# Kernel optimization log

Measured on AMD Instinct MI355X. Metric: run time of the kernel, lower is better.

## Reference

```python
import jax, jax.numpy as jnp
import numpy as np

IM_SIZE = (128, 128)  # N_i per image dim
N_BATCH, N_COILS, N_TRJ = 1, 8, 8192


def _image_grid(im_size):
    # r_i in [-1/2, 1/2): (arange(N_i) - N_i//2) / N_i, flattened to (R, d)
    axes = [(jnp.arange(n, dtype=jnp.float32) - n // 2) / n for n in im_size]
    mesh = jnp.meshgrid(*axes, indexing='ij')
    return jnp.stack([m.reshape(-1) for m in mesh], axis=-1)  # (R, d)


def setup_inputs() -> dict:
    key = jax.random.key(0)
    k1, k2, k3 = jax.random.split(key, 3)
    img_real = jax.random.normal(k1, (N_BATCH, N_COILS) + IM_SIZE, dtype=jnp.float32)
    img_imag = jax.random.normal(k2, (N_BATCH, N_COILS) + IM_SIZE, dtype=jnp.float32)
    # trajectory k_i uniform in [-N_i/2, N_i/2]
    scale = jnp.asarray(IM_SIZE, dtype=jnp.float32)
    trj = (jax.random.uniform(k3, (N_BATCH, N_TRJ, len(IM_SIZE)), dtype=jnp.float32) - 0.5) * scale
    return {"img_real": img_real, "img_imag": img_imag, "trj": trj}


def reference(img_real, img_imag, trj):
    # matrix_nufft.forward: ksp[n,c,k] = sum_r img[n,c,r] * exp(-j 2 pi k . r)
    d = trj.shape[-1]
    im_size = img_real.shape[-d:]
    grid = _image_grid(im_size)                              # (R, d)
    phase = jnp.einsum('nkd,rd->nkr', trj, grid)             # (N, K, R)
    A = jnp.exp(-2j * jnp.pi * phase)                        # (N, K, R) complex64
    img = (img_real + 1j * img_imag).reshape(img_real.shape[0], -1, grid.shape[0])  # (N, C, R)
    ksp = jnp.einsum('nkr,ncr->nck', A, img)                 # (N, C, K) complex64
    # return real/imag stacked on last axis (harness-friendly real output)
    return jnp.stack([ksp.real, ksp.imag], axis=-1)          # (N, C, K, 2)
```

## Files before the change

### kernel.cpp

```cpp
#include <hip/hip_runtime.h>
#include <math.h>


#define K_TOTAL 8192
#define KB      64
#define NX      128
#define NY      128

typedef short  bf16x8 __attribute__((ext_vector_type(8)));
typedef float  f32x4  __attribute__((ext_vector_type(4)));

__device__ inline unsigned short f32_to_bf16_rne(float f) {
    unsigned int u = __float_as_uint(f);
    u += 0x7FFFu + ((u >> 16) & 1u);
    return (unsigned short)(u >> 16);
}
__device__ inline unsigned pack2(float a, float b) {
    return (unsigned)f32_to_bf16_rne(a) | ((unsigned)f32_to_bf16_rne(b) << 16);
}

__global__ __launch_bounds__(512, 1) void nufft_mfma_kernel(
    const float* __restrict__ imgR,
    const float* __restrict__ imgI,
    const float* __restrict__ trj,
    float* __restrict__ out)
{
    __shared__ __align__(16) unsigned short slab[2][2][128 * 128];

    const int tid = threadIdx.x;
    const int bid = blockIdx.x;
    const int cg  = bid >> 7;
    const int kg0 = (bid & 127) * KB;
    const int c0  = cg * 2;

    const int wave = tid >> 6;
    const int lane = tid & 63;
    const int l15  = lane & 15;
    const int lg   = lane >> 4;
    const int c2   = wave & 1;
    const int kq   = wave >> 1;
    const int c    = c0 + c2;

    const int rowgrp = tid >> 5;
    const int seg    = tid & 31;

    {
        float4 L0[4], L1[4];
        const float* bR0 = imgR + (c0 * NX) * NY + seg * 4;
        const float* bI0 = imgI + (c0 * NX) * NY + seg * 4;
        const float* bR1 = imgR + ((c0 + 1) * NX) * NY + seg * 4;
        const float* bI1 = imgI + ((c0 + 1) * NX) * NY + seg * 4;

        {
            const int row = rowgrp;
            L0[0] = *(const float4*)(bR0 + row * NY);
            L0[1] = *(const float4*)(bI0 + row * NY);
            L0[2] = *(const float4*)(bR1 + row * NY);
            L0[3] = *(const float4*)(bI1 + row * NY);
        }
#pragma unroll
        for (int i = 0; i < 8; ++i) {
            float4* cu = (i & 1) ? L1 : L0;
            float4* nx = (i & 1) ? L0 : L1;
            if (i < 7) {
                const int row = rowgrp + 16 * (i + 1);
                nx[0] = *(const float4*)(bR0 + row * NY);
                nx[1] = *(const float4*)(bI0 + row * NY);
                nx[2] = *(const float4*)(bR1 + row * NY);
                nx[3] = *(const float4*)(bI1 + row * NY);
            }
            const int row = rowgrp + 16 * i;
            const int off = row * 256 + ((seg * 8) ^ ((row & 15) << 4));
            uint2 v;
            v.x = pack2(cu[0].x, cu[0].y); v.y = pack2(cu[0].z, cu[0].w);
            *(uint2*)((char*)&slab[0][0][0] + off) = v;
            v.x = pack2(cu[1].x, cu[1].y); v.y = pack2(cu[1].z, cu[1].w);
            *(uint2*)((char*)&slab[0][1][0] + off) = v;
            v.x = pack2(cu[2].x, cu[2].y); v.y = pack2(cu[2].z, cu[2].w);
            *(uint2*)((char*)&slab[1][0][0] + off) = v;
            v.x = pack2(cu[3].x, cu[3].y); v.y = pack2(cu[3].z, cu[3].w);
            *(uint2*)((char*)&slab[1][1][0] + off) = v;
        }
    }

    bf16x8 aR[4], aI[4];
    {
        const float ky = trj[(kg0 + kq * 16 + l15) * 2 + 1];
        float u = -ky * (1.0f / 128.0f); u -= floorf(u);
        float s1i, s1r; __sincosf(6.283185307179586f * u, &s1i, &s1r);
#pragma unroll
        for (int ys = 0; ys < 4; ++ys) {
            const int y0 = ys * 32 + lg * 8;
            float t = -ky * (float)(y0 - 64) * (1.0f / 128.0f); t -= floorf(t);
            float ci_, cr_; __sincosf(6.283185307179586f * t, &ci_, &cr_);
#pragma unroll
            for (int m = 0; m < 8; ++m) {
                aR[ys][m] = (short)f32_to_bf16_rne(cr_);
                aI[ys][m] = (short)f32_to_bf16_rne(ci_);
                const float nr = cr_ * s1r - ci_ * s1i;
                ci_ = cr_ * s1i + ci_ * s1r;
                cr_ = nr;
            }
        }
    }

    float kxv[4];
#pragma unroll
    for (int j = 0; j < 4; ++j)
        kxv[j] = trj[(kg0 + kq * 16 + lg * 4 + j) * 2 + 0];

    __syncthreads();

    const char* sbR = (const char*)&slab[c2][0][0];
    const char* sbI = (const char*)&slab[c2][1][0];

    f32x4 outRe = {0,0,0,0};
    f32x4 outIm = {0,0,0,0};

#pragma unroll
    for (int nt = 0; nt < 8; ++nt) {
        const int x    = nt * 16 + l15;
        const int rowb = x * 256;

        f32x4 P = {0,0,0,0}, Q = {0,0,0,0}, U = {0,0,0,0}, V = {0,0,0,0};
#pragma unroll
        for (int ys = 0; ys < 4; ++ys) {
            const int inb = (lg * 16 + ys * 64) ^ (l15 << 4);
            const bf16x8 bR = *(const bf16x8*)(sbR + rowb + inb);
            const bf16x8 bI = *(const bf16x8*)(sbI + rowb + inb);
            P = __builtin_amdgcn_mfma_f32_16x16x32_bf16(aR[ys], bR, P, 0, 0, 0);
            Q = __builtin_amdgcn_mfma_f32_16x16x32_bf16(aI[ys], bI, Q, 0, 0, 0);
            U = __builtin_amdgcn_mfma_f32_16x16x32_bf16(aR[ys], bI, U, 0, 0, 0);
            V = __builtin_amdgcn_mfma_f32_16x16x32_bf16(aI[ys], bR, V, 0, 0, 0);
        }

        const float rx = (float)(x - 64) * (1.0f / 128.0f);
#pragma unroll
        for (int j = 0; j < 4; ++j) {
            float t = -kxv[j] * rx; t -= floorf(t);
            float eI_, eR_; __sincosf(6.283185307179586f * t, &eI_, &eR_);
            const float TR = P[j] - Q[j];
            const float TI = U[j] + V[j];
            outRe[j] += eR_ * TR - eI_ * TI;
            outIm[j] += eR_ * TI + eI_ * TR;
        }
    }

#pragma unroll
    for (int j = 0; j < 4; ++j) {
        float r_ = outRe[j];
        float i_ = outIm[j];
#pragma unroll
        for (int m = 1; m < 16; m <<= 1) {
            r_ += __shfl_xor(r_, m, 64);
            i_ += __shfl_xor(i_, m, 64);
        }
        if (l15 == 0) {
            const int kg = kg0 + kq * 16 + lg * 4 + j;
            ((float2*)out)[c * K_TOTAL + kg] = make_float2(r_, i_);
        }
    }
}

extern "C" void kernel_launch(void* const* d_in, const int* in_sizes, int n_in,
                              void* d_out, int out_size, void* d_ws, size_t ws_size,
                              hipStream_t stream) {
    const float* imgR = (const float*)d_in[0];
    const float* imgI = (const float*)d_in[1];
    const float* trj  = (const float*)d_in[2];
    float* out = (float*)d_out;

    hipLaunchKernelGGL(nufft_mfma_kernel, dim3(512), dim3(512), 0, stream,
                       imgR, imgI, trj, out);
}
```

Baseline: 22.40 us.

## Double k-points per block to reuse staged image slab across two MFMA tiles

Each block now handles 128 k-samples instead of 64, and each wave computes two 16-row k tiles that share the same LDS B-fragments. The grid halves to 256 blocks. This amortizes the global-to-LDS image staging and bf16 conversion over twice the work and reuses each LDS read for two MFMAs. In exchange it doubles accumulator and A-fragment registers per wave, and 256 blocks may underfill the 256 CUs if occupancy per CU is one block.

```diff
diff --git a/kernel.cpp b/kernel.cpp
--- a/kernel.cpp
+++ b/kernel.cpp
@@ -3,7 +3,7 @@
 
 
 #define K_TOTAL 8192
-#define KB      64
+#define KB      128
 #define NX      128
 #define NY      128
 
@@ -29,8 +29,8 @@
 
     const int tid = threadIdx.x;
     const int bid = blockIdx.x;
-    const int cg  = bid >> 7;
-    const int kg0 = (bid & 127) * KB;
+    const int cg  = bid >> 6;
+    const int kg0 = (bid & 63) * KB;
     const int c0  = cg * 2;
 
     const int wave = tid >> 6;
@@ -83,9 +83,10 @@
         }
     }
 
-    bf16x8 aR[4], aI[4];
-    {
-        const float ky = trj[(kg0 + kq * 16 + l15) * 2 + 1];
+    bf16x8 aR[2][4], aI[2][4];
+#pragma unroll
+    for (int kt = 0; kt < 2; ++kt) {
+        const float ky = trj[(kg0 + kq * 32 + kt * 16 + l15) * 2 + 1];
         float u = -ky * (1.0f / 128.0f); u -= floorf(u);
         float s1i, s1r; __sincosf(6.283185307179586f * u, &s1i, &s1r);
 #pragma unroll
@@ -95,8 +96,8 @@
             float ci_, cr_; __sincosf(6.283185307179586f * t, &ci_, &cr_);
 #pragma unroll
             for (int m = 0; m < 8; ++m) {
-                aR[ys][m] = (short)f32_to_bf16_rne(cr_);
-                aI[ys][m] = (short)f32_to_bf16_rne(ci_);
+                aR[kt][ys][m] = (short)f32_to_bf16_rne(cr_);
+                aI[kt][ys][m] = (short)f32_to_bf16_rne(ci_);
                 const float nr = cr_ * s1r - ci_ * s1i;
                 ci_ = cr_ * s1i + ci_ * s1r;
                 cr_ = nr;
@@ -104,60 +105,74 @@
         }
     }
 
-    float kxv[4];
+    float kxv[2][4];
 #pragma unroll
-    for (int j = 0; j < 4; ++j)
-        kxv[j] = trj[(kg0 + kq * 16 + lg * 4 + j) * 2 + 0];
+    for (int kt = 0; kt < 2; ++kt)
+#pragma unroll
+        for (int j = 0; j < 4; ++j)
+            kxv[kt][j] = trj[(kg0 + kq * 32 + kt * 16 + lg * 4 + j) * 2 + 0];
 
     __syncthreads();
 
     const char* sbR = (const char*)&slab[c2][0][0];
     const char* sbI = (const char*)&slab[c2][1][0];
 
-    f32x4 outRe = {0,0,0,0};
-    f32x4 outIm = {0,0,0,0};
+    f32x4 outRe[2] = {{0,0,0,0},{0,0,0,0}};
+    f32x4 outIm[2] = {{0,0,0,0},{0,0,0,0}};
 
 #pragma unroll
     for (int nt = 0; nt < 8; ++nt) {
         const int x    = nt * 16 + l15;
         const int rowb = x * 256;
 
-        f32x4 P = {0,0,0,0}, Q = {0,0,0,0}, U = {0,0,0,0}, V = {0,0,0,0};
+        f32x4 P[2] = {{0,0,0,0},{0,0,0,0}};
+        f32x4 Q[2] = {{0,0,0,0},{0,0,0,0}};
+        f32x4 U[2] = {{0,0,0,0},{0,0,0,0}};
+        f32x4 V[2] = {{0,0,0,0},{0,0,0,0}};
 #pragma unroll
         for (int ys = 0; ys < 4; ++ys) {
             const int inb = (lg * 16 + ys * 64) ^ (l15 << 4);
             const bf16x8 bR = *(const bf16x8*)(sbR + rowb + inb);
             const bf16x8 bI = *(const bf16x8*)(sbI + rowb + inb);
-            P = __builtin_amdgcn_mfma_f32_16x16x32_bf16(aR[ys], bR, P, 0, 0, 0);
-            Q = __builtin_amdgcn_mfma_f32_16x16x32_bf16(aI[ys], bI, Q, 0, 0, 0);
-            U = __builtin_amdgcn_mfma_f32_16x16x32_bf16(aR[ys], bI, U, 0, 0, 0);
-            V = __builtin_amdgcn_mfma_f32_16x16x32_bf16(aI[ys], bR, V, 0, 0, 0);
+#pragma unroll
+            for (int kt = 0; kt < 2; ++kt) {
+                P[kt] = __builtin_amdgcn_mfma_f32_16x16x32_bf16(aR[kt][ys], bR, P[kt], 0, 0, 0);
+                Q[kt] = __builtin_amdgcn_mfma_f32_16x16x32_bf16(aI[kt][ys], bI, Q[kt], 0, 0, 0);
+                U[kt] = __builtin_amdgcn_mfma_f32_16x16x32_bf16(aR[kt][ys], bI, U[kt], 0, 0, 0);
+                V[kt] = __builtin_amdgcn_mfma_f32_16x16x32_bf16(aI[kt][ys], bR, V[kt], 0, 0, 0);
+            }
         }
 
         const float rx = (float)(x - 64) * (1.0f / 128.0f);
 #pragma unroll
-        for (int j = 0; j < 4; ++j) {
-            float t = -kxv[j] * rx; t -= floorf(t);
-            float eI_, eR_; __sincosf(6.283185307179586f * t, &eI_, &eR_);
-            const float TR = P[j] - Q[j];
-            const float TI = U[j] + V[j];
-            outRe[j] += eR_ * TR - eI_ * TI;
-            outIm[j] += eR_ * TI + eI_ * TR;
+        for (int kt = 0; kt < 2; ++kt) {
+#pragma unroll
+            for (int j = 0; j < 4; ++j) {
+                float t = -kxv[kt][j] * rx; t -= floorf(t);
+                float eI_, eR_; __sincosf(6.283185307179586f * t, &eI_, &eR_);
+                const float TR = P[kt][j] - Q[kt][j];
+                const float TI = U[kt][j] + V[kt][j];
+                outRe[kt][j] += eR_ * TR - eI_ * TI;
+                outIm[kt][j] += eR_ * TI + eI_ * TR;
+            }
         }
     }
 
 #pragma unroll
-    for (int j = 0; j < 4; ++j) {
-        float r_ = outRe[j];
-        float i_ = outIm[j];
+    for (int kt = 0; kt < 2; ++kt) {
 #pragma unroll
-        for (int m = 1; m < 16; m <<= 1) {
-            r_ += __shfl_xor(r_, m, 64);
-            i_ += __shfl_xor(i_, m, 64);
-        }
-        if (l15 == 0) {
-            const int kg = kg0 + kq * 16 + lg * 4 + j;
-            ((float2*)out)[c * K_TOTAL + kg] = make_float2(r_, i_);
+        for (int j = 0; j < 4; ++j) {
+            float r_ = outRe[kt][j];
+            float i_ = outIm[kt][j];
+#pragma unroll
+            for (int m = 1; m < 16; m <<= 1) {
+                r_ += __shfl_xor(r_, m, 64);
+                i_ += __shfl_xor(i_, m, 64);
+            }
+            if (l15 == 0) {
+                const int kg = kg0 + kq * 32 + kt * 16 + lg * 4 + j;
+                ((float2*)out)[c * K_TOTAL + kg] = make_float2(r_, i_);
+            }
         }
     }
 }
@@ -170,6 +185,6 @@
     const float* trj  = (const float*)d_in[2];
     float* out = (float*)d_out;
 
-    hipLaunchKernelGGL(nufft_mfma_kernel, dim3(512), dim3(512), 0, stream,
+    hipLaunchKernelGGL(nufft_mfma_kernel, dim3(256), dim3(512), 0, stream,
                        imgR, imgI, trj, out);
 }
```

After: 57.50 us. 157% more time.

## Assign one coil per block with 128 k-points to halve LDS and raise occupancy

Applied to the files above, without the earlier changes.

Each block now handles a single coil and 128 trajectory points, with all 8 waves sharing one coil slab, instead of two coils and 64 points split across waves. The LDS footprint drops from 128KB to 64KB and launch bounds now allow two blocks per CU, so image staging can overlap compute in another block. Each block still loads and converts a full coil image, so total staging work per k-point is unchanged. The grid remains 512 blocks, but the per-thread register budget is tighter.

```diff
diff --git a/kernel.cpp b/kernel.cpp
--- a/kernel.cpp
+++ b/kernel.cpp
@@ -3,7 +3,7 @@
 
 
 #define K_TOTAL 8192
-#define KB      64
+#define KB      128
 #define NX      128
 #define NY      128
 
@@ -19,73 +19,59 @@
     return (unsigned)f32_to_bf16_rne(a) | ((unsigned)f32_to_bf16_rne(b) << 16);
 }
 
-__global__ __launch_bounds__(512, 1) void nufft_mfma_kernel(
+__global__ __launch_bounds__(512, 2) void nufft_mfma_kernel(
     const float* __restrict__ imgR,
     const float* __restrict__ imgI,
     const float* __restrict__ trj,
     float* __restrict__ out)
 {
-    __shared__ __align__(16) unsigned short slab[2][2][128 * 128];
+    __shared__ __align__(16) unsigned short slab[2][128 * 128];
 
     const int tid = threadIdx.x;
     const int bid = blockIdx.x;
-    const int cg  = bid >> 7;
-    const int kg0 = (bid & 127) * KB;
-    const int c0  = cg * 2;
+    const int c   = bid >> 6;
+    const int kg0 = (bid & 63) * KB;
 
     const int wave = tid >> 6;
     const int lane = tid & 63;
     const int l15  = lane & 15;
     const int lg   = lane >> 4;
-    const int c2   = wave & 1;
-    const int kq   = wave >> 1;
-    const int c    = c0 + c2;
 
     const int rowgrp = tid >> 5;
     const int seg    = tid & 31;
 
     {
-        float4 L0[4], L1[4];
-        const float* bR0 = imgR + (c0 * NX) * NY + seg * 4;
-        const float* bI0 = imgI + (c0 * NX) * NY + seg * 4;
-        const float* bR1 = imgR + ((c0 + 1) * NX) * NY + seg * 4;
-        const float* bI1 = imgI + ((c0 + 1) * NX) * NY + seg * 4;
+        float4 R0, I0, R1, I1;
+        const float* bR = imgR + (c * NX) * NY + seg * 4;
+        const float* bI = imgI + (c * NX) * NY + seg * 4;
 
-        {
-            const int row = rowgrp;
-            L0[0] = *(const float4*)(bR0 + row * NY);
-            L0[1] = *(const float4*)(bI0 + row * NY);
-            L0[2] = *(const float4*)(bR1 + row * NY);
-            L0[3] = *(const float4*)(bI1 + row * NY);
-        }
+        R0 = *(const float4*)(bR + rowgrp * NY);
+        I0 = *(const float4*)(bI + rowgrp * NY);
 #pragma unroll
         for (int i = 0; i < 8; ++i) {
-            float4* cu = (i & 1) ? L1 : L0;
-            float4* nx = (i & 1) ? L0 : L1;
+            const bool even = (i & 1) == 0;
             if (i < 7) {
-                const int row = rowgrp + 16 * (i + 1);
-                nx[0] = *(const float4*)(bR0 + row * NY);
-                nx[1] = *(const float4*)(bI0 + row * NY);
-                nx[2] = *(const float4*)(bR1 + row * NY);
-                nx[3] = *(const float4*)(bI1 + row * NY);
+                const int rown = rowgrp + 16 * (i + 1);
+                if (even) { R1 = *(const float4*)(bR + rown * NY);
+                            I1 = *(const float4*)(bI + rown * NY); }
+                else      { R0 = *(const float4*)(bR + rown * NY);
+                            I0 = *(const float4*)(bI + rown * NY); }
             }
+            const float4 vR = even ? R0 : R1;
+            const float4 vI = even ? I0 : I1;
             const int row = rowgrp + 16 * i;
             const int off = row * 256 + ((seg * 8) ^ ((row & 15) << 4));
             uint2 v;
-            v.x = pack2(cu[0].x, cu[0].y); v.y = pack2(cu[0].z, cu[0].w);
-            *(uint2*)((char*)&slab[0][0][0] + off) = v;
-            v.x = pack2(cu[1].x, cu[1].y); v.y = pack2(cu[1].z, cu[1].w);
-            *(uint2*)((char*)&slab[0][1][0] + off) = v;
-            v.x = pack2(cu[2].x, cu[2].y); v.y = pack2(cu[2].z, cu[2].w);
-            *(uint2*)((char*)&slab[1][0][0] + off) = v;
-            v.x = pack2(cu[3].x, cu[3].y); v.y = pack2(cu[3].z, cu[3].w);
-            *(uint2*)((char*)&slab[1][1][0] + off) = v;
+            v.x = pack2(vR.x, vR.y); v.y = pack2(vR.z, vR.w);
+            *(uint2*)((char*)&slab[0][0] + off) = v;
+            v.x = pack2(vI.x, vI.y); v.y = pack2(vI.z, vI.w);
+            *(uint2*)((char*)&slab[1][0] + off) = v;
         }
     }
 
     bf16x8 aR[4], aI[4];
     {
-        const float ky = trj[(kg0 + kq * 16 + l15) * 2 + 1];
+        const float ky = trj[(kg0 + wave * 16 + l15) * 2 + 1];
         float u = -ky * (1.0f / 128.0f); u -= floorf(u);
         float s1i, s1r; __sincosf(6.283185307179586f * u, &s1i, &s1r);
 #pragma unroll
@@ -107,12 +93,12 @@
     float kxv[4];
 #pragma unroll
     for (int j = 0; j < 4; ++j)
-        kxv[j] = trj[(kg0 + kq * 16 + lg * 4 + j) * 2 + 0];
+        kxv[j] = trj[(kg0 + wave * 16 + lg * 4 + j) * 2 + 0];
 
     __syncthreads();
 
-    const char* sbR = (const char*)&slab[c2][0][0];
-    const char* sbI = (const char*)&slab[c2][1][0];
+    const char* sbR = (const char*)&slab[0][0];
+    const char* sbI = (const char*)&slab[1][0];
 
     f32x4 outRe = {0,0,0,0};
     f32x4 outIm = {0,0,0,0};
@@ -156,7 +142,7 @@
             i_ += __shfl_xor(i_, m, 64);
         }
         if (l15 == 0) {
-            const int kg = kg0 + kq * 16 + lg * 4 + j;
+            const int kg = kg0 + wave * 16 + lg * 4 + j;
             ((float2*)out)[c * K_TOTAL + kg] = make_float2(r_, i_);
         }
     }
```

New measurement: 20.89 us, median of 2. 1.07x faster.
